# Kernel tuning notes

Hardware: AMD Instinct MI355X
Metric: run time of the kernel (lower is better)

The kernel has to match this reference:

```python
import jax, jax.numpy as jnp
import numpy as np

N_NODES = 100000
N_EDGES = 1600000
HID = 128
HEADS = 8
DK = HID // HEADS
N_LAYERS = 4
IN_DIM = 32
N_CLASSES = 16


def _ln(x, g, b, eps=1e-5):
    mu = x.mean(-1, keepdims=True)
    var = x.var(-1, keepdims=True)
    return (x - mu) / jnp.sqrt(var + eps) * g + b


def setup_inputs() -> dict:
    key = jax.random.key(0)
    ks = jax.random.split(key, 24)
    s = 0.05
    inp = {
        'feat': jax.random.randint(ks[0], (N_NODES,), 0, IN_DIM, dtype=jnp.int32),
        'edge_src': jax.random.randint(ks[1], (N_EDGES,), 0, N_NODES, dtype=jnp.int32),
        'edge_dst': jnp.sort(jax.random.randint(ks[2], (N_EDGES,), 0, N_NODES, dtype=jnp.int32)),
        'emb': jax.random.normal(ks[3], (IN_DIM, HID), jnp.float32) * s,
        'Wq': jax.random.normal(ks[4], (N_LAYERS, HID, HID), jnp.float32) * s,
        'Wk': jax.random.normal(ks[5], (N_LAYERS, HID, HID), jnp.float32) * s,
        'Wv': jax.random.normal(ks[6], (N_LAYERS, HID, HID), jnp.float32) * s,
        'Wo': jax.random.normal(ks[7], (N_LAYERS, HID, HID), jnp.float32) * s,
        'bo': jnp.zeros((N_LAYERS, HID), jnp.float32),
        'ln1_g': jnp.ones((N_LAYERS, HID), jnp.float32),
        'ln1_b': jnp.zeros((N_LAYERS, HID), jnp.float32),
        'W1': jax.random.normal(ks[8], (N_LAYERS, HID, 2 * HID), jnp.float32) * s,
        'b1': jnp.zeros((N_LAYERS, 2 * HID), jnp.float32),
        'W2': jax.random.normal(ks[9], (N_LAYERS, 2 * HID, HID), jnp.float32) * s,
        'b2': jnp.zeros((N_LAYERS, HID), jnp.float32),
        'ln2_g': jnp.ones((N_LAYERS, HID), jnp.float32),
        'ln2_b': jnp.zeros((N_LAYERS, HID), jnp.float32),
        'mW0': jax.random.normal(ks[10], (HID, HID // 2), jnp.float32) * s,
        'mb0': jnp.zeros((HID // 2,), jnp.float32),
        'mW1': jax.random.normal(ks[11], (HID // 2, HID // 4), jnp.float32) * s,
        'mb1': jnp.zeros((HID // 4,), jnp.float32),
        'mW2': jax.random.normal(ks[12], (HID // 4, N_CLASSES), jnp.float32) * s,
        'mb2': jnp.zeros((N_CLASSES,), jnp.float32),
    }
    return inp


def reference(feat, edge_src, edge_dst, emb, Wq, Wk, Wv, Wo, bo, ln1_g, ln1_b,
              W1, b1, W2, b2, ln2_g, ln2_b, mW0, mb0, mW1, mb1, mW2, mb2):
    N = feat.shape[0]
    h = emb[feat]  # [N, HID] embedding gather
    inv_sqrt_dk = jnp.float32(1.0 / np.sqrt(DK))
    for l in range(Wq.shape[0]):
        h_in1 = h
        q = (h @ Wq[l]).reshape(N, HEADS, DK)
        k = (h @ Wk[l]).reshape(N, HEADS, DK)
        v = (h @ Wv[l]).reshape(N, HEADS, DK)
        # per-edge scores: K[src] . Q[dst], scaled, clipped, exponentiated
        sc = jnp.einsum('ehd,ehd->eh', k[edge_src], q[edge_dst]) * inv_sqrt_dk
        sc = jnp.exp(jnp.clip(sc, -5.0, 5.0))  # [E, HEADS]
        wV = jax.ops.segment_sum(sc[:, :, None] * v[edge_src], edge_dst, num_segments=N)
        z = jax.ops.segment_sum(sc, edge_dst, num_segments=N)
        attn = (wV / (z[:, :, None] + 1e-6)).reshape(N, HID)
        h = h_in1 + (attn @ Wo[l] + bo[l])  # residual + O proj
        h = _ln(h, ln1_g[l], ln1_b[l])
        h_in2 = h
        f = jax.nn.relu(h @ W1[l] + b1[l]) @ W2[l] + b2[l]
        h = _ln(h_in2 + f, ln2_g[l], ln2_b[l])
    # MLPReadout: HID -> HID/2 -> HID/4 -> n_classes
    h = jax.nn.relu(h @ mW0 + mb0)
    h = jax.nn.relu(h @ mW1 + mb1)
    return h @ mW2 + mb2
```

## Files before the change

### kernel.cpp

```cpp
#include <hip/hip_runtime.h>
#include <hip/hip_fp16.h>

#define HID 128
#define N_LAYERS 4
#define IN_DIM 32
#define N_CLASSES 16

typedef _Float16 f16x8 __attribute__((ext_vector_type(8)));
typedef float f32x2 __attribute__((ext_vector_type(2)));
typedef __attribute__((ext_vector_type(4))) float f32x4;
typedef unsigned int uint_t;

#if defined(__has_builtin)
#if __has_builtin(__builtin_amdgcn_cvt_pk_f32_fp8)
#define HAVE_CVT_FP8 1
#endif
#if __has_builtin(__builtin_amdgcn_cvt_pk_fp8_f32)
#define HAVE_ENC_FP8 1
#endif
#endif

__device__ __forceinline__ unsigned short f2bf(float f) {
    unsigned int u = __float_as_uint(f);
    return (unsigned short)((u + 0x7FFFu + ((u >> 16) & 1u)) >> 16);
}
__device__ __forceinline__ float2 up16(uint_t u) {
    __half2 h = *(__half2*)&u;
    return __half22float2(h);
}

__device__ __forceinline__ unsigned char f2e4m3(float f) {
    unsigned int u = __float_as_uint(f);
    unsigned char s = (unsigned char)((u >> 24) & 0x80u);
    unsigned int a = u & 0x7FFFFFFFu;
    if (a >= 0x43E00000u) return s | 0x7Eu;
    int exp = (int)(a >> 23) - 127;
    if (exp < -6) {
        int m = (int)rintf(__uint_as_float(a) * 512.f);
        return s | (unsigned char)m;
    }
    unsigned int lsb = (a >> 20) & 1u;
    a += 0x7FFFFu + lsb;
    int e8 = ((int)(a >> 23) - 127) + 7;
    unsigned int m8 = (a >> 20) & 7u;
    return s | (unsigned char)((e8 << 3) | (int)m8);
}
__device__ __forceinline__ float e4m32f(unsigned int b) {
    unsigned int s = (b & 0x80u) << 24;
    unsigned int E = (b >> 3) & 15u, m = b & 7u;
    if (E == 0) {
        float v = (float)m * 0.001953125f;
        return __uint_as_float(__float_as_uint(v) | s);
    }
    return __uint_as_float(s | ((E + 120u) << 23) | (m << 20));
}
__device__ __forceinline__ unsigned char enc8(float v) {
#ifdef HAVE_ENC_FP8
    int r = __builtin_amdgcn_cvt_pk_fp8_f32(v, v, 0, false);
    return (unsigned char)(r & 0xFF);
#else
    return f2e4m3(v);
#endif
}
__device__ __forceinline__ void dec8v(uint_t u, f32x2* o) {
#ifdef HAVE_CVT_FP8
    o[0] = __builtin_amdgcn_cvt_pk_f32_fp8(u, false);
    o[1] = __builtin_amdgcn_cvt_pk_f32_fp8(u, true);
#else
    o[0] = (f32x2){e4m32f(u & 255u), e4m32f((u >> 8) & 255u)};
    o[1] = (f32x2){e4m32f((u >> 16) & 255u), e4m32f(u >> 24)};
#endif
}

__device__ __forceinline__ int frag_off(int row, int c) {
    return ((c >> 5) << 10) + (((c >> 3) & 3) << 8) + (row << 4) + ((c & 7) << 1);
}

__global__ void detect_kernel(const unsigned int* __restrict__ ln1g, int* __restrict__ flag) {
    if (threadIdx.x == 0 && blockIdx.x == 0)
        *flag = (ln1g[0] == 0x3F800000u) ? 0 : 1;
}

#define NSM 11
struct SArgs {
    const void* src[NSM];
    float*      dst[NSM];
    int         cnt[NSM];
};

__global__ void conv_kernel(SArgs args, const int* __restrict__ flag) {
    int p = blockIdx.y;
    int n = args.cnt[p];
    int base = (blockIdx.x * 256 + threadIdx.x) * 4;
    if (base >= n) return;
    float* dst = args.dst[p];
    if (*flag) {
        const unsigned short* s = (const unsigned short*)args.src[p];
        #pragma unroll
        for (int j = 0; j < 4; ++j)
            dst[base + j] = __uint_as_float(((unsigned int)s[base + j]) << 16);
    } else {
        const float* s = (const float*)args.src[p];
        *(float4*)&dst[base] = *(const float4*)&s[base];
    }
}

#define NW 27
struct WArgs {
    const void* src[NW];
    int         soff[NW];
    _Float16*   dst[NW];
    int         K[NW];
    int         M[NW];
    int         mode[NW];
};

__global__ void wconv_kernel(WArgs a, const int* __restrict__ flag) {
    int p = blockIdx.y;
    int K = a.K[p], M = a.M[p], mode = a.mode[p];
    int idx = blockIdx.x * 256 + threadIdx.x;
    if (idx >= K * M) return;
    int k = idx / M, m = idx % M;
    float v;
    if (*flag)
        v = __uint_as_float(((unsigned int)((const unsigned short*)a.src[p])[a.soff[p] + idx]) << 16);
    else
        v = ((const float*)a.src[p])[a.soff[p] + idx];
    size_t off;
    if (mode == 0) {
        off = (size_t)m * K + k;
    } else {
        int ht, k2;
        if (mode == 1) { ht = m >> 5; k2 = k; }
        else           { ht = ((k >> 7) << 2) + (m >> 5); k2 = k & 127; }
        int frag = (((k2 >> 5) * 2 + ((m >> 4) & 1)) << 6) + (((k2 >> 3) & 3) << 4) + (m & 15);
        off = (size_t)ht * 4096 + frag * 8 + (k & 7);
    }
    a.dst[p][off] = (_Float16)v;
}

__global__ void csr_kernel(const int* __restrict__ dst, int* __restrict__ row_start,
                           int N, int E) {
    int n = blockIdx.x * 256 + threadIdx.x;
    if (n > N) return;
    int lo = 0, hi = E;
    while (lo < hi) {
        int mid = (lo + hi) >> 1;
        if (dst[mid] < n) lo = mid + 1; else hi = mid;
    }
    row_start[n] = lo;
}

__global__ void embed_kernel(const int* __restrict__ feat, const float* __restrict__ emb,
                             _Float16* __restrict__ h, int N) {
    int idx = blockIdx.x * 256 + threadIdx.x;
    if (idx >= N * 16) return;
    int n  = idx >> 4;
    int c8 = idx & 15;
    int f = feat[n];
    const float* s = &emb[(size_t)f * HID + c8 * 8];
    float4 a = *(const float4*)s;
    float4 b = *(const float4*)(s + 4);
    f16x8 o;
    o[0] = (_Float16)a.x; o[1] = (_Float16)a.y; o[2] = (_Float16)a.z; o[3] = (_Float16)a.w;
    o[4] = (_Float16)b.x; o[5] = (_Float16)b.y; o[6] = (_Float16)b.z; o[7] = (_Float16)b.w;
    *(f16x8*)&h[(size_t)n * HID + c8 * 8] = o;
}

__launch_bounds__(256)
__global__ void mfma_gemm_qkv(const _Float16* __restrict__ Ain,
                              const _Float16* __restrict__ Bt,
                              _Float16* __restrict__ q16, unsigned char* __restrict__ kvp8) {
    __shared__ __align__(16) char As[16384];
    __shared__ __align__(16) char Bs[49152];

    const int t    = threadIdx.x;
    const int w    = t >> 6;
    const int l    = t & 63;
    const int quad = l >> 4;
    const int lc   = l & 15;
    const int row0 = blockIdx.x * 64;
    const int mbase = blockIdx.y * 192;

    char* Aw = As + (w << 12);

    #pragma unroll
    for (int i = 0; i < 4; ++i) {
        int idx = i * 64 + l;
        int row = idx >> 4, g = idx & 15;
        uint4 v = *(const uint4*)(Ain + (size_t)(row0 + w * 16 + row) * 128 + g * 8);
        *(uint4*)(Aw + ((g >> 2) << 10) + ((g & 3) << 8) + (row << 4)) = v;
    }
    {
        const uint4* Bsrc = (const uint4*)(Bt + (size_t)(mbase / 32) * 4096);
        #pragma unroll
        for (int i = 0; i < 12; ++i) {
            int idx = t + i * 256;
            *(uint4*)&Bs[idx * 16] = Bsrc[idx];
        }
    }
    __syncthreads();

    f32x4 acc[12];
    #pragma unroll
    for (int i = 0; i < 12; ++i) acc[i] = (f32x4){0.f, 0.f, 0.f, 0.f};

    #pragma unroll
    for (int kk = 0; kk < 4; ++kk) {
        f16x8 af = *(const f16x8*)(Aw + (kk << 10) + (quad << 8) + (lc << 4));
        #pragma unroll
        for (int i = 0; i < 12; ++i) {
            f16x8 bf = *(const f16x8*)(Bs + (i >> 1) * 8192 +
                                       ((kk * 2 + (i & 1)) << 10) + (quad << 8) + (lc << 4));
            acc[i] = __builtin_amdgcn_mfma_f32_16x16x32_f16(af, bf, acc[i], 0, 0, 0);
        }
    }

    #pragma unroll
    for (int r = 0; r < 4; ++r) {
        int row = row0 + w * 16 + quad * 4 + r;
        #pragma unroll
        for (int i = 0; i < 12; ++i) {
            float v = acc[i][r];
            int gc = mbase + i * 16 + lc;
            if (gc < 128)      q16[(size_t)row * 128 + gc] = (_Float16)v;
            else if (gc < 256) kvp8[(size_t)row * 256 + (gc - 128)] = enc8(v);
            else               kvp8[(size_t)row * 256 + 128 + (gc - 256)] = enc8(v);
        }
    }
}

template<int NEXTM, bool RMODE>
__launch_bounds__(256, 3)
__global__ void layer_tail_fused(const _Float16* __restrict__ t2, _Float16* __restrict__ h,
                                 const _Float16* __restrict__ Wo, const _Float16* __restrict__ W1,
                                 const _Float16* __restrict__ W2,
                                 const _Float16* __restrict__ Wn, const float* __restrict__ bn,
                                 const float* __restrict__ bo,  const float* __restrict__ l1g,
                                 const float* __restrict__ l1b, const float* __restrict__ b1,
                                 const float* __restrict__ b2,  const float* __restrict__ l2g,
                                 const float* __restrict__ l2b,
                                 _Float16* __restrict__ q16, unsigned char* __restrict__ kvp8) {
    constexpr int NHT = NEXTM / 32;
    __shared__ __align__(16) char bufA[16384];
    __shared__ __align__(16) char bufH[16384];
    __shared__ __align__(16) char bufB[16384];

    const int t = threadIdx.x, w = t >> 6, l = t & 63;
    const int quad = l >> 4, lc = l & 15;
    const int row0 = blockIdx.x * 64;
    char* Aw = bufA + (w << 12);
    char* Hw = bufH + (w << 12);

    auto ISSUE = [&](const _Float16* src, int bsel) {
        char* d = bufB + bsel * 8192 + w * 2048;
        const char* g = (const char*)src + w * 2048 + l * 16;
        __builtin_amdgcn_global_load_lds(
            (const __attribute__((address_space(1))) unsigned int*)g,
            (__attribute__((address_space(3))) unsigned int*)d, 16, 0, 0);
        __builtin_amdgcn_global_load_lds(
            (const __attribute__((address_space(1))) unsigned int*)(g + 1024),
            (__attribute__((address_space(3))) unsigned int*)(d + 1024), 16, 0, 0);
    };
    auto MF2 = [&](const char* Ar, int bsel, f32x4* ac) {
        const char* B = bufB + bsel * 8192;
        #pragma unroll
        for (int kk = 0; kk < 4; ++kk) {
            f16x8 af = *(const f16x8*)(Ar + (kk << 10) + (quad << 8) + (lc << 4));
            #pragma unroll
            for (int i = 0; i < 2; ++i) {
                f16x8 bf = *(const f16x8*)(B + ((kk * 2 + i) << 10) + (quad << 8) + (lc << 4));
                ac[i] = __builtin_amdgcn_mfma_f32_16x16x32_f16(af, bf, ac[i], 0, 0, 0);
            }
        }
    };

    ISSUE(Wo, 0);

    _Float16 resv[4][8];
    #pragma unroll
    for (int r = 0; r < 4; ++r) {
        int row = row0 + w * 16 + quad * 4 + r;
        #pragma unroll
        for (int j = 0; j < 8; ++j)
            resv[r][j] = h[(size_t)row * 128 + j * 16 + lc];
    }

    #pragma unroll
    for (int i = 0; i < 4; ++i) {
        int idx = i * 64 + l;
        int row = idx >> 4, g = idx & 15;
        uint4 v = *(const uint4*)(t2 + (size_t)(row0 + w * 16 + row) * 128 + g * 8);
        *(uint4*)(Aw + ((g >> 2) << 10) + ((g & 3) << 8) + (row << 4)) = v;
    }

    __syncthreads();
    int bb = 0;

    f32x4 acc[8];
    #pragma unroll
    for (int i = 0; i < 8; ++i) acc[i] = (f32x4){0.f, 0.f, 0.f, 0.f};
    #pragma unroll
    for (int c = 0; c < 4; ++c) {
        ISSUE(c < 3 ? Wo + (c + 1) * 4096 : W1, bb ^ 1);
        MF2(Aw, bb, acc + c * 2);
        __syncthreads();
        bb ^= 1;
    }

    {
        float gv[8], bv[8], bb8[8];
        #pragma unroll
        for (int j = 0; j < 8; ++j) {
            int col = j * 16 + lc;
            gv[j] = l1g[col]; bv[j] = l1b[col]; bb8[j] = bo[col];
        }
        #pragma unroll
        for (int r = 0; r < 4; ++r) {
            float v[8];
            float s = 0.f, ss = 0.f;
            #pragma unroll
            for (int j = 0; j < 8; ++j) {
                v[j] = acc[j][r] + bb8[j] + (float)resv[r][j];
                s += v[j]; ss += v[j] * v[j];
            }
            #pragma unroll
            for (int m = 1; m <= 8; m <<= 1) { s += __shfl_xor(s, m); ss += __shfl_xor(ss, m); }
            float mu   = s * (1.f / 128.f);
            float rstd = rsqrtf(ss * (1.f / 128.f) - mu * mu + 1e-5f);
            #pragma unroll
            for (int j = 0; j < 8; ++j) {
                float o = (v[j] - mu) * rstd * gv[j] + bv[j];
                *(_Float16*)(Hw + frag_off(quad * 4 + r, j * 16 + lc)) = (_Float16)o;
            }
        }
    }

    f32x4 acc3[8];
    #pragma unroll
    for (int i = 0; i < 8; ++i) acc3[i] = (f32x4){0.f, 0.f, 0.f, 0.f};
    #pragma unroll
    for (int hh = 0; hh < 2; ++hh) {
        #pragma unroll
        for (int j = 0; j < 4; ++j) {
            ISSUE(j < 3 ? W1 + (hh * 4 + j + 1) * 4096 : W2 + (hh * 4) * 4096, bb ^ 1);
            f32x4 a2[2];
            a2[0] = (f32x4){0.f, 0.f, 0.f, 0.f};
            a2[1] = (f32x4){0.f, 0.f, 0.f, 0.f};
            MF2(Hw, bb, a2);
            #pragma unroll
            for (int r = 0; r < 4; ++r) {
                #pragma unroll
                for (int i2 = 0; i2 < 2; ++i2) {
                    float v = a2[i2][r] + b1[(hh * 4 + j) * 32 + i2 * 16 + lc];
                    v = fmaxf(v, 0.f);
                    *(_Float16*)(Aw + frag_off(quad * 4 + r, j * 32 + i2 * 16 + lc)) = (_Float16)v;
                }
            }
            __syncthreads();
            bb ^= 1;
        }
        #pragma unroll
        for (int j = 0; j < 4; ++j) {
            const _Float16* nxt;
            if (j < 3)          nxt = W2 + (hh * 4 + j + 1) * 4096;
            else if (hh == 0)   nxt = W1 + 4 * 4096;
            else                nxt = Wn;
            ISSUE(nxt, bb ^ 1);
            MF2(Aw, bb, acc3 + j * 2);
            __syncthreads();
            bb ^= 1;
        }
    }

    f16x8 ov[4];
    {
        float gv[8], bv[8], bb8[8];
        #pragma unroll
        for (int j = 0; j < 8; ++j) {
            int col = j * 16 + lc;
            gv[j] = l2g[col]; bv[j] = l2b[col]; bb8[j] = b2[col];
        }
        #pragma unroll
        for (int r = 0; r < 4; ++r) {
            float v[8];
            float s = 0.f, ss = 0.f;
            #pragma unroll
            for (int j = 0; j < 8; ++j) {
                float res = (float)*(const _Float16*)(Hw + frag_off(quad * 4 + r, j * 16 + lc));
                v[j] = acc3[j][r] + bb8[j] + res;
                s += v[j]; ss += v[j] * v[j];
            }
            #pragma unroll
            for (int m = 1; m <= 8; m <<= 1) { s += __shfl_xor(s, m); ss += __shfl_xor(ss, m); }
            float mu   = s * (1.f / 128.f);
            float rstd = rsqrtf(ss * (1.f / 128.f) - mu * mu + 1e-5f);
            #pragma unroll
            for (int j = 0; j < 8; ++j) {
                float o = (v[j] - mu) * rstd * gv[j] + bv[j];
                ov[r][j] = (_Float16)o;
                *(_Float16*)(Aw + frag_off(quad * 4 + r, j * 16 + lc)) = (_Float16)o;
            }
        }
    }

    auto storeP = [&](int p, const f32x4* pf) {
        #pragma unroll
        for (int r = 0; r < 4; ++r) {
            int row = row0 + w * 16 + quad * 4 + r;
            #pragma unroll
            for (int i2 = 0; i2 < 2; ++i2) {
                int gc = p * 32 + i2 * 16 + lc;
                float v = pf[i2][r];
                if (RMODE) {
                    v += bn[gc];
                    v = fmaxf(v, 0.f);
                    q16[(size_t)row * 64 + gc] = (_Float16)v;
                } else {
                    if (gc < 128)      q16[(size_t)row * 128 + gc] = (_Float16)v;
                    else if (gc < 256) kvp8[(size_t)row * 256 + (gc - 128)] = enc8(v);
                    else               kvp8[(size_t)row * 256 + 128 + (gc - 256)] = enc8(v);
                }
            }
        }
    };

    f32x4 pf[2];
    #pragma unroll
    for (int c = 0; c < NHT; ++c) {
        if (c + 1 < NHT) ISSUE(Wn + (c + 1) * 4096, bb ^ 1);
        if (c == 0) {
            #pragma unroll
            for (int r = 0; r < 4; ++r) {
                int row = row0 + w * 16 + quad * 4 + r;
                #pragma unroll
                for (int j = 0; j < 8; ++j)
                    h[(size_t)row * 128 + j * 16 + lc] = ov[r][j];
            }
        } else {
            storeP(c - 1, pf);
        }
        f32x4 a4[2];
        a4[0] = (f32x4){0.f, 0.f, 0.f, 0.f};
        a4[1] = (f32x4){0.f, 0.f, 0.f, 0.f};
        MF2(Aw, bb, a4);
        if (c + 1 < NHT) __syncthreads();
        bb ^= 1;
        pf[0] = a4[0]; pf[1] = a4[1];
    }
    storeP(NHT - 1, pf);
}

__launch_bounds__(256)
__global__ void readout_tail(const _Float16* __restrict__ r0,
                             const _Float16* __restrict__ w1t, const float* __restrict__ b1_,
                             const _Float16* __restrict__ w2t, const float* __restrict__ b2_,
                             void* __restrict__ outp, const int* __restrict__ flag, int N) {
    constexpr int SA = 144;
    constexpr int SR = 80;
    __shared__ __align__(16) char bufA[64 * SA];
    __shared__ __align__(16) char bufR[64 * SR];

    const int t    = threadIdx.x;
    const int w    = t >> 6;
    const int l    = t & 63;
    const int quad = l >> 4;
    const int lc   = l & 15;
    const int row0 = blockIdx.x * 64;

    #pragma unroll
    for (int i = 0; i < 2; ++i) {
        int idx = t + i * 256;
        int r = idx >> 3, u = idx & 7;
        *(uint4*)&bufA[r * SA + u * 16] = *(const uint4*)(r0 + (size_t)(row0 + r) * 64 + u * 8);
    }
    __syncthreads();

    f32x4 acc[2];
    acc[0] = (f32x4){0.f, 0.f, 0.f, 0.f};
    acc[1] = (f32x4){0.f, 0.f, 0.f, 0.f};
    #pragma unroll
    for (int kk = 0; kk < 2; ++kk) {
        f16x8 af = *(const f16x8*)&bufA[(w * 16 + lc) * SA + kk * 64 + quad * 16];
        #pragma unroll
        for (int i = 0; i < 2; ++i) {
            f16x8 bf = *(const f16x8*)(w1t + (size_t)(i * 16 + lc) * 64 + kk * 32 + quad * 8);
            acc[i] = __builtin_amdgcn_mfma_f32_16x16x32_f16(af, bf, acc[i], 0, 0, 0);
        }
    }
    #pragma unroll
    for (int r = 0; r < 4; ++r) {
        int lrow = (w * 16 + quad * 4 + r) * SR;
        #pragma unroll
        for (int i = 0; i < 2; ++i) {
            float v = acc[i][r] + b1_[i * 16 + lc];
            v = fmaxf(v, 0.f);
            *(_Float16*)&bufR[lrow + (i * 16 + lc) * 2] = (_Float16)v;
        }
    }
    __syncthreads();
    f32x4 a2 = (f32x4){0.f, 0.f, 0.f, 0.f};
    {
        f16x8 af = *(const f16x8*)&bufR[(w * 16 + lc) * SR + quad * 16];
        f16x8 bf = *(const f16x8*)(w2t + (size_t)lc * 32 + quad * 8);
        a2 = __builtin_amdgcn_mfma_f32_16x16x32_f16(af, bf, a2, 0, 0, 0);
    }
    #pragma unroll
    for (int r = 0; r < 4; ++r) {
        int row = row0 + w * 16 + quad * 4 + r;
        if (row < N) {
            float v = a2[r] + b2_[lc];
            size_t o = (size_t)row * 16 + lc;
            if (*flag) ((unsigned short*)outp)[o] = f2bf(v);
            else       ((float*)outp)[o] = v;
        }
    }
}

__global__ void attn_kernel(const _Float16* __restrict__ q16, const uint_t* __restrict__ kvp,
                            const int* __restrict__ esrc, const int* __restrict__ rows,
                            _Float16* __restrict__ out, int N) {
    int node = (blockIdx.x * blockDim.x + threadIdx.x) >> 6;
    if (node >= N) return;
    int l    = threadIdx.x & 63;
    int head = l & 7;
    int eg   = l >> 3;

    f32x2 qh[8];
    {
        const uint4* qp = (const uint4*)(q16 + (size_t)node * HID + head * 16);
        uint4 q0 = qp[0], q1 = qp[1];
        uint_t qs[8] = {q0.x, q0.y, q0.z, q0.w, q1.x, q1.y, q1.z, q1.w};
        #pragma unroll
        for (int i = 0; i < 8; ++i) {
            float2 f = up16(qs[i]);
            qh[i] = (f32x2){f.x * 0.25f, f.y * 0.25f};
        }
    }
    int e0 = rows[node], e1 = rows[node + 1];
    f32x2 wv[8];
    #pragma unroll
    for (int i = 0; i < 8; ++i) wv[i] = (f32x2){0.f, 0.f};
    float z = 0.f;

    for (int eb = e0; eb < e1; eb += 16) {
        int ea = eb + eg, ec = eb + 8 + eg;
        bool oka = ea < e1, okc = ec < e1;
        int sa  = esrc[oka ? ea : e1 - 1];
        int sc_ = esrc[okc ? ec : e1 - 1];
        uint4 ka = *(const uint4*)(kvp + (size_t)sa  * 64 + head * 4);
        uint4 va = *(const uint4*)(kvp + (size_t)sa  * 64 + 32 + head * 4);
        uint4 kc = *(const uint4*)(kvp + (size_t)sc_ * 64 + head * 4);
        uint4 vc = *(const uint4*)(kvp + (size_t)sc_ * 64 + 32 + head * 4);

        f32x2 k2a[8], k2c[8];
        dec8v(ka.x, k2a); dec8v(ka.y, k2a + 2); dec8v(ka.z, k2a + 4); dec8v(ka.w, k2a + 6);
        dec8v(kc.x, k2c); dec8v(kc.y, k2c + 2); dec8v(kc.z, k2c + 4); dec8v(kc.w, k2c + 6);
        f32x2 da2 = (f32x2){0.f, 0.f}, dc2 = (f32x2){0.f, 0.f};
        #pragma unroll
        for (int j = 0; j < 8; ++j) { da2 += qh[j] * k2a[j]; dc2 += qh[j] * k2c[j]; }
        float da = da2.x + da2.y, dc = dc2.x + dc2.y;
        float sa2 = oka ? __expf(fminf(fmaxf(da, -5.f), 5.f)) : 0.f;
        float sc2 = okc ? __expf(fminf(fmaxf(dc, -5.f), 5.f)) : 0.f;

        f32x2 v2a[8], v2c[8];
        dec8v(va.x, v2a); dec8v(va.y, v2a + 2); dec8v(va.z, v2a + 4); dec8v(va.w, v2a + 6);
        dec8v(vc.x, v2c); dec8v(vc.y, v2c + 2); dec8v(vc.z, v2c + 4); dec8v(vc.w, v2c + 6);
        f32x2 pa = (f32x2){sa2, sa2}, pc = (f32x2){sc2, sc2};
        #pragma unroll
        for (int j = 0; j < 8; ++j) { wv[j] += pa * v2a[j]; wv[j] += pc * v2c[j]; }
        z += sa2 + sc2;
    }
    #pragma unroll
    for (int m = 8; m < 64; m <<= 1) {
        z += __shfl_xor(z, m);
        #pragma unroll
        for (int i = 0; i < 8; ++i) {
            wv[i].x += __shfl_xor(wv[i].x, m);
            wv[i].y += __shfl_xor(wv[i].y, m);
        }
    }
    if (eg == 0) {
        float inv = 1.f / (z + 1e-6f);
        f16x8 o0, o1;
        #pragma unroll
        for (int i = 0; i < 4; ++i) {
            o0[2*i]   = (_Float16)(wv[i].x * inv);
            o0[2*i+1] = (_Float16)(wv[i].y * inv);
            o1[2*i]   = (_Float16)(wv[4+i].x * inv);
            o1[2*i+1] = (_Float16)(wv[4+i].y * inv);
        }
        *(f16x8*)&out[(size_t)node * HID + head * 16]     = o0;
        *(f16x8*)&out[(size_t)node * HID + head * 16 + 8] = o1;
    }
}

extern "C" void kernel_launch(void* const* d_in, const int* in_sizes, int n_in,
                              void* d_out, int out_size, void* d_ws, size_t ws_size,
                              hipStream_t stream) {
    const int N  = in_sizes[0];
    const int E  = in_sizes[1];
    const int RB = (N + 63) / 64;
    const size_t NP = (size_t)RB * 64;

    const int* d_feat = (const int*)d_in[0];
    const int* d_esrc = (const int*)d_in[1];
    const int* d_edst = (const int*)d_in[2];

    char* base = (char*)d_ws;
    size_t cur = 0;
    auto alloc = [&](size_t bytes) -> char* {
        cur = (cur + 255) & ~(size_t)255;
        char* p = base + cur;
        cur += bytes;
        return p;
    };
    int* d_flag = (int*)alloc(4);
    int* d_rows = (int*)alloc((size_t)(N + 1) * 4);

    float* p_emb = (float*)alloc(IN_DIM * HID * 4);
    float* p_bo  = (float*)alloc(N_LAYERS * HID * 4);
    float* p_l1g = (float*)alloc(N_LAYERS * HID * 4);
    float* p_l1b = (float*)alloc(N_LAYERS * HID * 4);
    float* p_b1  = (float*)alloc(N_LAYERS * 2 * HID * 4);
    float* p_b2  = (float*)alloc(N_LAYERS * HID * 4);
    float* p_l2g = (float*)alloc(N_LAYERS * HID * 4);
    float* p_l2b = (float*)alloc(N_LAYERS * HID * 4);
    float* p_mb0 = (float*)alloc(64 * 4);
    float* p_mb1 = (float*)alloc(32 * 4);
    float* p_mb2 = (float*)alloc(16 * 4);

    _Float16* wqkv_t = (_Float16*)alloc((size_t)N_LAYERS * 384 * 128 * 2);
    _Float16* wo_t   = (_Float16*)alloc((size_t)N_LAYERS * 128 * 128 * 2);
    _Float16* w1_t   = (_Float16*)alloc((size_t)N_LAYERS * 256 * 128 * 2);
    _Float16* w2_t   = (_Float16*)alloc((size_t)N_LAYERS * 128 * 256 * 2);
    _Float16* mw0_t  = (_Float16*)alloc(64 * 128 * 2);
    _Float16* mw1_t  = (_Float16*)alloc(32 * 64 * 2);
    _Float16* mw2_t  = (_Float16*)alloc(16 * 32 * 2);

    _Float16*      buf_h = (_Float16*)alloc(NP * HID * 2);
    _Float16*      q16   = (_Float16*)alloc(NP * HID * 2);
    _Float16*      t2    = (_Float16*)alloc(NP * HID * 2);
    unsigned char* kvp   = (unsigned char*)alloc(NP * 256);

    detect_kernel<<<1, 64, 0, stream>>>((const unsigned int*)d_in[9], d_flag);

    {
        SArgs sa;
        const int sidx[NSM] = {3, 8, 9, 10, 12, 14, 15, 16, 18, 20, 22};
        float*    sdst[NSM] = {p_emb, p_bo, p_l1g, p_l1b, p_b1, p_b2, p_l2g, p_l2b, p_mb0, p_mb1, p_mb2};
        const int scnt[NSM] = {IN_DIM*HID, N_LAYERS*HID, N_LAYERS*HID, N_LAYERS*HID,
                               N_LAYERS*2*HID, N_LAYERS*HID, N_LAYERS*HID, N_LAYERS*HID, 64, 32, 16};
        for (int i = 0; i < NSM; ++i) { sa.src[i] = d_in[sidx[i]]; sa.dst[i] = sdst[i]; sa.cnt[i] = scnt[i]; }
        conv_kernel<<<dim3(4, NSM), 256, 0, stream>>>(sa, d_flag);
    }

    {
        WArgs wa;
        int wi = 0;
        auto addw = [&](int inp, int off, int Kd, int Md, _Float16* dst, int mode) {
            wa.src[wi] = d_in[inp]; wa.soff[wi] = off; wa.K[wi] = Kd; wa.M[wi] = Md;
            wa.dst[wi] = dst; wa.mode[wi] = mode; ++wi;
        };
        for (int l = 0; l < N_LAYERS; ++l) {
            addw(4,  l * 16384, 128, 128, wqkv_t + (size_t)l * 49152, 1);
            addw(5,  l * 16384, 128, 128, wqkv_t + (size_t)l * 49152 + 16384, 1);
            addw(6,  l * 16384, 128, 128, wqkv_t + (size_t)l * 49152 + 32768, 1);
            addw(7,  l * 16384, 128, 128, wo_t + (size_t)l * 16384, 1);
            addw(11, l * 32768, 128, 256, w1_t + (size_t)l * 32768, 1);
            addw(13, l * 32768, 256, 128, w2_t + (size_t)l * 32768, 2);
        }
        addw(17, 0, 128, 64, mw0_t, 1);
        addw(19, 0, 64,  32, mw1_t, 0);
        addw(21, 0, 32,  16, mw2_t, 0);
        wconv_kernel<<<dim3(128, NW), 256, 0, stream>>>(wa, d_flag);
    }

    csr_kernel<<<(N + 1 + 255) / 256, 256, 0, stream>>>(d_edst, d_rows, N, E);
    embed_kernel<<<((size_t)N * 16 + 255) / 256, 256, 0, stream>>>(d_feat, p_emb, buf_h, N);

    const int GBW = (N + 3) / 4;

    mfma_gemm_qkv<<<dim3(RB, 2), 256, 0, stream>>>(buf_h, wqkv_t, q16, kvp);

    for (int l = 0; l < N_LAYERS; ++l) {
        const _Float16* Wo = wo_t + (size_t)l * 16384;
        const _Float16* W1 = w1_t + (size_t)l * 32768;
        const _Float16* W2 = w2_t + (size_t)l * 32768;
        const float* bo  = p_bo  + (size_t)l * HID;
        const float* l1g = p_l1g + (size_t)l * HID;
        const float* l1b = p_l1b + (size_t)l * HID;
        const float* b1  = p_b1  + (size_t)l * 2 * HID;
        const float* b2  = p_b2  + (size_t)l * HID;
        const float* l2g = p_l2g + (size_t)l * HID;
        const float* l2b = p_l2b + (size_t)l * HID;

        attn_kernel<<<GBW, 256, 0, stream>>>(q16, (const uint_t*)kvp, d_esrc, d_rows, t2, N);

        if (l < N_LAYERS - 1) {
            layer_tail_fused<384, false><<<RB, 256, 0, stream>>>(
                t2, buf_h, Wo, W1, W2, wqkv_t + (size_t)(l + 1) * 49152, nullptr,
                bo, l1g, l1b, b1, b2, l2g, l2b, q16, kvp);
        } else {
            layer_tail_fused<64, true><<<RB, 256, 0, stream>>>(
                t2, buf_h, Wo, W1, W2, mw0_t, p_mb0,
                bo, l1g, l1b, b1, b2, l2g, l2b, q16, nullptr);
        }
    }

    readout_tail<<<RB, 256, 0, stream>>>(q16, mw1_t, p_mb1, mw2_t, p_mb2, d_out, d_flag, N);
}
```

Baseline: 818.6 us.

## Assign one 8-lane group per node in attention with software-pipelined edge loads

The attention kernel now maps 8 lanes (one per head) to each node instead of a full 64-lane wavefront, so each wave handles 8 nodes. Each lane walks all of its node's edges two at a time, prefetching the next pair's K/V while computing the current pair. The cross-lane shuffle reduction goes away, and lanes no longer sit idle on low-degree nodes (average degree is 16). In exchange, per-lane latency chains get longer, load balance depends on per-node degree within a wave, and gathers are spread across 8 different nodes per wave.

```diff
diff --git a/kernel.cpp b/kernel.cpp
--- a/kernel.cpp
+++ b/kernel.cpp
@@ -520,11 +520,10 @@
 __global__ void attn_kernel(const _Float16* __restrict__ q16, const uint_t* __restrict__ kvp,
                             const int* __restrict__ esrc, const int* __restrict__ rows,
                             _Float16* __restrict__ out, int N) {
-    int node = (blockIdx.x * blockDim.x + threadIdx.x) >> 6;
+    int gid  = blockIdx.x * blockDim.x + threadIdx.x;
+    int node = gid >> 3;
     if (node >= N) return;
-    int l    = threadIdx.x & 63;
-    int head = l & 7;
-    int eg   = l >> 3;
+    int head = threadIdx.x & 7;
 
     f32x2 qh[8];
     {
@@ -543,56 +542,60 @@
     for (int i = 0; i < 8; ++i) wv[i] = (f32x2){0.f, 0.f};
     float z = 0.f;
 
-    for (int eb = e0; eb < e1; eb += 16) {
-        int ea = eb + eg, ec = eb + 8 + eg;
-        bool oka = ea < e1, okc = ec < e1;
-        int sa  = esrc[oka ? ea : e1 - 1];
-        int sc_ = esrc[okc ? ec : e1 - 1];
-        uint4 ka = *(const uint4*)(kvp + (size_t)sa  * 64 + head * 4);
-        uint4 va = *(const uint4*)(kvp + (size_t)sa  * 64 + 32 + head * 4);
-        uint4 kc = *(const uint4*)(kvp + (size_t)sc_ * 64 + head * 4);
-        uint4 vc = *(const uint4*)(kvp + (size_t)sc_ * 64 + 32 + head * 4);
-
+    uint4 ka = {0,0,0,0}, va = {0,0,0,0}, kc = {0,0,0,0}, vc = {0,0,0,0};
+    bool oka = e0 < e1, okc = e0 + 1 < e1;
+    if (oka) {
+        int sa = esrc[e0];
+        int sc = okc ? esrc[e0 + 1] : sa;
+        ka = *(const uint4*)(kvp + (size_t)sa * 64 + head * 4);
+        va = *(const uint4*)(kvp + (size_t)sa * 64 + 32 + head * 4);
+        kc = *(const uint4*)(kvp + (size_t)sc * 64 + head * 4);
+        vc = *(const uint4*)(kvp + (size_t)sc * 64 + 32 + head * 4);
+    }
+
+    for (int e = e0; e < e1; e += 2) {
+        uint4 cka = ka, cva = va, ckc = kc, cvc = vc;
+        bool coka = oka, cokc = okc;
+        int en = e + 2;
+        oka = en < e1; okc = en + 1 < e1;
+        if (oka) {
+            int sa = esrc[en];
+            int sc = okc ? esrc[en + 1] : sa;
+            ka = *(const uint4*)(kvp + (size_t)sa * 64 + head * 4);
+            va = *(const uint4*)(kvp + (size_t)sa * 64 + 32 + head * 4);
+            kc = *(const uint4*)(kvp + (size_t)sc * 64 + head * 4);
+            vc = *(const uint4*)(kvp + (size_t)sc * 64 + 32 + head * 4);
+        }
         f32x2 k2a[8], k2c[8];
-        dec8v(ka.x, k2a); dec8v(ka.y, k2a + 2); dec8v(ka.z, k2a + 4); dec8v(ka.w, k2a + 6);
-        dec8v(kc.x, k2c); dec8v(kc.y, k2c + 2); dec8v(kc.z, k2c + 4); dec8v(kc.w, k2c + 6);
+        dec8v(cka.x, k2a); dec8v(cka.y, k2a + 2); dec8v(cka.z, k2a + 4); dec8v(cka.w, k2a + 6);
+        dec8v(ckc.x, k2c); dec8v(ckc.y, k2c + 2); dec8v(ckc.z, k2c + 4); dec8v(ckc.w, k2c + 6);
         f32x2 da2 = (f32x2){0.f, 0.f}, dc2 = (f32x2){0.f, 0.f};
         #pragma unroll
         for (int j = 0; j < 8; ++j) { da2 += qh[j] * k2a[j]; dc2 += qh[j] * k2c[j]; }
         float da = da2.x + da2.y, dc = dc2.x + dc2.y;
-        float sa2 = oka ? __expf(fminf(fmaxf(da, -5.f), 5.f)) : 0.f;
-        float sc2 = okc ? __expf(fminf(fmaxf(dc, -5.f), 5.f)) : 0.f;
+        float sa2 = coka ? __expf(fminf(fmaxf(da, -5.f), 5.f)) : 0.f;
+        float sc2 = cokc ? __expf(fminf(fmaxf(dc, -5.f), 5.f)) : 0.f;
 
         f32x2 v2a[8], v2c[8];
-        dec8v(va.x, v2a); dec8v(va.y, v2a + 2); dec8v(va.z, v2a + 4); dec8v(va.w, v2a + 6);
-        dec8v(vc.x, v2c); dec8v(vc.y, v2c + 2); dec8v(vc.z, v2c + 4); dec8v(vc.w, v2c + 6);
+        dec8v(cva.x, v2a); dec8v(cva.y, v2a + 2); dec8v(cva.z, v2a + 4); dec8v(cva.w, v2a + 6);
+        dec8v(cvc.x, v2c); dec8v(cvc.y, v2c + 2); dec8v(cvc.z, v2c + 4); dec8v(cvc.w, v2c + 6);
         f32x2 pa = (f32x2){sa2, sa2}, pc = (f32x2){sc2, sc2};
         #pragma unroll
         for (int j = 0; j < 8; ++j) { wv[j] += pa * v2a[j]; wv[j] += pc * v2c[j]; }
         z += sa2 + sc2;
     }
-    #pragma unroll
-    for (int m = 8; m < 64; m <<= 1) {
-        z += __shfl_xor(z, m);
-        #pragma unroll
-        for (int i = 0; i < 8; ++i) {
-            wv[i].x += __shfl_xor(wv[i].x, m);
-            wv[i].y += __shfl_xor(wv[i].y, m);
-        }
-    }
-    if (eg == 0) {
-        float inv = 1.f / (z + 1e-6f);
-        f16x8 o0, o1;
-        #pragma unroll
-        for (int i = 0; i < 4; ++i) {
-            o0[2*i]   = (_Float16)(wv[i].x * inv);
-            o0[2*i+1] = (_Float16)(wv[i].y * inv);
-            o1[2*i]   = (_Float16)(wv[4+i].x * inv);
-            o1[2*i+1] = (_Float16)(wv[4+i].y * inv);
-        }
-        *(f16x8*)&out[(size_t)node * HID + head * 16]     = o0;
-        *(f16x8*)&out[(size_t)node * HID + head * 16 + 8] = o1;
-    }
+
+    float inv = 1.f / (z + 1e-6f);
+    f16x8 o0, o1;
+    #pragma unroll
+    for (int i = 0; i < 4; ++i) {
+        o0[2*i]   = (_Float16)(wv[i].x * inv);
+        o0[2*i+1] = (_Float16)(wv[i].y * inv);
+        o1[2*i]   = (_Float16)(wv[4+i].x * inv);
+        o1[2*i+1] = (_Float16)(wv[4+i].y * inv);
+    }
+    *(f16x8*)&out[(size_t)node * HID + head * 16]     = o0;
+    *(f16x8*)&out[(size_t)node * HID + head * 16 + 8] = o1;
 }
 
 extern "C" void kernel_launch(void* const* d_in, const int* in_sizes, int n_in,
@@ -679,7 +682,7 @@
     csr_kernel<<<(N + 1 + 255) / 256, 256, 0, stream>>>(d_edst, d_rows, N, E);
     embed_kernel<<<((size_t)N * 16 + 255) / 256, 256, 0, stream>>>(d_feat, p_emb, buf_h, N);
 
-    const int GBW = (N + 3) / 4;
+    const int GBW = ((size_t)N * 8 + 255) / 256;
 
     mfma_gemm_qkv<<<dim3(RB, 2), 256, 0, stream>>>(buf_h, wqkv_t, q16, kvp);
 
```

New measurement: 751.8 us. 1.09x faster.
